# Performance work log

Hardware: AMD Instinct MI355X
Metric: run time of the kernel (lower is better)

The kernel has to match this reference:

```python
import jax, jax.numpy as jnp
from jax import lax
import numpy as np

B = 262144
CLASSES = 11


def setup_inputs() -> dict:
    key = jax.random.key(0)
    ks = jax.random.split(key, 8)
    exponents = jax.random.randint(ks[0], (B, 16), 0, CLASSES, dtype=jnp.int32)
    conv0_w = jax.random.normal(ks[1], (4, 12, 1, 2), jnp.float32) * 0.1
    conv0_b = jax.random.normal(ks[2], (4,), jnp.float32) * 0.05
    conv1_w = jax.random.normal(ks[3], (4, 12, 2, 1), jnp.float32) * 0.1
    # xavier-uniform linears, bias filled with 0.01 (as in init_weights)
    lim1 = float(np.sqrt(6.0 / (96 + 256)))
    linear_w = jax.random.uniform(ks[4], (256, 96), jnp.float32, -lim1, lim1)
    linear_b = jnp.full((256,), 0.01, jnp.float32)
    lim2 = float(np.sqrt(6.0 / (256 + 4)))
    out_w = jax.random.uniform(ks[5], (4, 256), jnp.float32, -lim2, lim2)
    out_b = jnp.full((4,), 0.01, jnp.float32)
    return {"exponents": exponents, "conv0_w": conv0_w, "conv0_b": conv0_b,
            "conv1_w": conv1_w, "linear_w": linear_w, "linear_b": linear_b,
            "out_w": out_w, "out_b": out_b}


def _conv(x, w):
    return lax.conv_general_dilated(x, w, (1, 1), 'VALID',
                                    dimension_numbers=('NCHW', 'OIHW', 'NCHW'))


def _forward(exponents, conv0_w, conv0_b, conv1_w, linear_w, linear_b, out_w, out_b):
    e = exponents.reshape(-1, 4, 4)
    # reconstruct board values: 0 tile stays 0, else 2**e
    x = jnp.where(e == 0, 0.0, jnp.exp2(e.astype(jnp.float32)))  # [B,4,4]
    # rotate_normalize: flips chosen from argmax corner (computed BEFORE flipping)
    corners = jnp.stack([x[:, 0, 0], x[:, 0, -1], x[:, -1, 0], x[:, -1, -1]], axis=1)
    ix = jnp.argmax(corners, axis=1)
    flip_v = ix >= 2          # floor(ix/2) == 1
    flip_h = (ix % 2) == 1
    x = jnp.where(flip_v[:, None, None], x[:, ::-1, :], x)
    x = jnp.where(flip_h[:, None, None], x[:, :, ::-1], x)
    # log2 with 0 -> 0, one-hot over 11 classes
    x_log = jnp.log2(x + (x == 0).astype(jnp.float32))
    onehot = jax.nn.one_hot(jnp.round(x_log).astype(jnp.int32), CLASSES,
                            dtype=jnp.float32)          # [B,4,4,11]
    onehot = jnp.transpose(onehot, (0, 3, 1, 2))         # [B,11,4,4]
    mask = onehot.sum(axis=1, keepdims=True)             # channel 0 (all ones)
    feat = jnp.concatenate([mask, onehot], axis=1)       # [B,12,4,4]
    zh = jax.nn.relu(_conv(feat, conv0_w) + conv0_b[None, :, None, None])  # [B,4,4,3]
    zv = jax.nn.relu(_conv(feat, conv1_w))                                  # [B,4,3,4]
    z1 = jnp.concatenate([zh.reshape(-1, 48), zv.reshape(-1, 48)], axis=1)  # [B,96]
    z2 = jax.nn.relu(z1 @ linear_w.T + linear_b)                            # [B,256]
    probs = jax.nn.softmax(z2 @ out_w.T + out_b, axis=1)                    # [B,4]
    # unscramble: vert swaps actions (0,1); horiz swaps actions (2,3)
    perm = jnp.stack([jnp.where(flip_v, 1, 0), jnp.where(flip_v, 0, 1),
                      jnp.where(flip_h, 3, 2), jnp.where(flip_h, 2, 3)], axis=1)
    return jnp.take_along_axis(probs, perm, axis=1)


def reference(exponents, conv0_w, conv0_b, conv1_w, linear_w, linear_b, out_w, out_b):
    return _forward(exponents, conv0_w, conv0_b, conv1_w, linear_w, linear_b, out_w, out_b)
```

## Files before the change

### kernel.cpp

```cpp
#include <hip/hip_runtime.h>

typedef unsigned int  u32;
typedef unsigned short u16;

typedef float    f4  __attribute__((ext_vector_type(4)));
typedef short    bf8 __attribute__((ext_vector_type(8)));
typedef __fp16   h8  __attribute__((ext_vector_type(8)));
typedef __fp16   h2  __attribute__((ext_vector_type(2)));

#define NBLK  1024
#define ITERS 4
#define ZSTR  104

__device__ __forceinline__ u32 bfr(float f) {
    union { float f; u32 u; } v; v.f = f;
    return (v.u + 0x8000u) >> 16;
}
__device__ __forceinline__ u32 pk2(float lo, float hi) { return bfr(lo) | (bfr(hi) << 16); }
__device__ __forceinline__ u32 pkh(float lo, float hi) {
    union { h2 h; u32 u; } v; v.h = __builtin_amdgcn_cvt_pkrtz(lo, hi); return v.u;
}
__device__ __forceinline__ u32 nrev(u32 x) {
    return ((x >> 12) & 0xFu) | ((x >> 4) & 0xF0u) | ((x << 4) & 0xF00u) | ((x << 12) & 0xF000u);
}

__device__ __forceinline__ void phase1_fn(const int4 e4, u16* __restrict__ z1b, u32* __restrict__ flgb,
                                          const uint2* __restrict__ Th, const uint2* __restrict__ Tv,
                                          const int w, const int m, const int qd)
{
    u32 pkd = (u32)e4.x | ((u32)e4.y << 4) | ((u32)e4.z << 8) | ((u32)e4.w << 12);
    u32 R0 = (u32)__shfl((int)pkd, m);
    u32 R1 = (u32)__shfl((int)pkd, m + 16);
    u32 R2 = (u32)__shfl((int)pkd, m + 32);
    u32 R3 = (u32)__shfl((int)pkd, m + 48);
    u32 c0v = R0 & 15u, c1v = (R0 >> 12) & 15u, c2v = R3 & 15u, c3v = (R3 >> 12) & 15u;
    u32 best = c0v; int ix = 0;
    if (c1v > best) { best = c1v; ix = 1; }
    if (c2v > best) { best = c2v; ix = 2; }
    if (c3v > best) { best = c3v; ix = 3; }
    const bool fv = (ix >= 2), fh = ((ix & 1) != 0);
    u32 F[4];
    F[0] = fv ? R3 : R0;
    F[1] = fv ? R2 : R1;
    F[2] = fv ? R1 : R2;
    F[3] = fv ? R0 : R3;
    #pragma unroll
    for (int i = 0; i < 4; ++i) F[i] = fh ? nrev(F[i]) : F[i];

    if (qd == 0) flgb[w*16 + m] = (u32)fv | ((u32)fh << 1);

    const u32 Fq = F[qd];
    u32 nbq[4], nbc[4];
    #pragma unroll
    for (int j = 0; j < 4; ++j) nbq[j] = (Fq >> (4*j)) & 15u;
    #pragma unroll
    for (int i = 0; i < 4; ++i) nbc[i] = (F[i] >> (4*qd)) & 15u;

    uint2 H0 = Th[nbq[0]*11u + nbq[1]];
    uint2 H1 = Th[nbq[1]*11u + nbq[2]];
    uint2 H2 = Th[nbq[2]*11u + nbq[3]];
    uint2 V0 = Tv[nbc[0]*11u + nbc[1]];
    uint2 V1 = Tv[nbc[1]*11u + nbc[2]];
    uint2 V2 = Tv[nbc[2]*11u + nbc[3]];

    u16* zrow = &z1b[(w*16 + m) * ZSTR];
    *(uint2*)(zrow + (qd*3 + 0)*4) = H0;
    *(uint2*)(zrow + (qd*3 + 1)*4) = H1;
    *(uint2*)(zrow + (qd*3 + 2)*4) = H2;
    *(uint2*)(zrow + 48 + (0*4 + qd)*4) = V0;
    *(uint2*)(zrow + 48 + (1*4 + qd)*4) = V1;
    *(uint2*)(zrow + 48 + (2*4 + qd)*4) = V2;
}

__device__ __forceinline__ void gemm_fn(const u16* __restrict__ z1b, float4* __restrict__ Pb,
                                        const bf8 (&af)[4][3], const u32 (&owA)[2][4], const f4 (&lb4)[4],
                                        const int w, const int m, const int qd)
{
    #pragma unroll
    for (int G = 0; G < 4; ++G) {
        bf8 zb[3];
        #pragma unroll
        for (int s = 0; s < 3; ++s)
            zb[s] = *(const bf8*)(&z1b[(G*16 + m)*ZSTR + s*32 + qd*8]);

        f4 acc_t[4] = {lb4[0], lb4[1], lb4[2], lb4[3]};
        #pragma unroll
        for (int s = 0; s < 3; ++s)
            #pragma unroll
            for (int tt = 0; tt < 4; ++tt)
                acc_t[tt] = __builtin_amdgcn_mfma_f32_16x16x32_bf16(af[tt][s], zb[s], acc_t[tt], 0, 0, 0);

        f4 acc2 = {0.f, 0.f, 0.f, 0.f};
        #pragma unroll
        for (int c = 0; c < 2; ++c) {
            union { u32 u[4]; h8 v; } bu, au;
            bu.u[0] = pkh(fmaxf(acc_t[2*c  ][0], 0.f), fmaxf(acc_t[2*c  ][1], 0.f));
            bu.u[1] = pkh(fmaxf(acc_t[2*c  ][2], 0.f), fmaxf(acc_t[2*c  ][3], 0.f));
            bu.u[2] = pkh(fmaxf(acc_t[2*c+1][0], 0.f), fmaxf(acc_t[2*c+1][1], 0.f));
            bu.u[3] = pkh(fmaxf(acc_t[2*c+1][2], 0.f), fmaxf(acc_t[2*c+1][3], 0.f));
            au.u[0] = owA[c][0]; au.u[1] = owA[c][1]; au.u[2] = owA[c][2]; au.u[3] = owA[c][3];
            acc2 = __builtin_amdgcn_mfma_f32_16x16x32_f16(au.v, bu.v, acc2, 0, 0, 0);
        }
        if (qd == 0)
            Pb[(G*4 + w)*16 + m] = make_float4(acc2[0], acc2[1], acc2[2], acc2[3]);
    }
}

__device__ __forceinline__ void epi_fn(const float4* __restrict__ Pb, const u32 fl, const float4 obv,
                                       float* __restrict__ out, const int base, const int m, const int qd)
{
    float4 s0 = Pb[(qd*4 + 0)*16 + m], s1 = Pb[(qd*4 + 1)*16 + m];
    float4 s2 = Pb[(qd*4 + 2)*16 + m], s3 = Pb[(qd*4 + 3)*16 + m];
    float L0 = s0.x + s1.x + s2.x + s3.x + obv.x;
    float L1 = s0.y + s1.y + s2.y + s3.y + obv.y;
    float L2 = s0.z + s1.z + s2.z + s3.z + obv.z;
    float L3 = s0.w + s1.w + s2.w + s3.w + obv.w;
    float mx = fmaxf(fmaxf(L0, L1), fmaxf(L2, L3));
    float e0 = __expf(L0 - mx), e1 = __expf(L1 - mx), e2 = __expf(L2 - mx), e3 = __expf(L3 - mx);
    float inv = __builtin_amdgcn_rcpf(e0 + e1 + e2 + e3);
    float p0 = e0 * inv, p1 = e1 * inv, p2 = e2 * inv, p3 = e3 * inv;
    float4 o;
    o.x = (fl & 1u) ? p1 : p0;
    o.y = (fl & 1u) ? p0 : p1;
    o.z = (fl & 2u) ? p3 : p2;
    o.w = (fl & 2u) ? p2 : p3;
    *(float4*)(out + (size_t)(base + qd*16 + m) * 4) = o;
}

__launch_bounds__(256, 4)
__global__ void smartcnn_fused(const int* __restrict__ exps,
                               const float* __restrict__ c0w, const float* __restrict__ c0b,
                               const float* __restrict__ c1w,
                               const float* __restrict__ lw,  const float* __restrict__ lb,
                               const float* __restrict__ ow,  const float* __restrict__ ob,
                               float* __restrict__ out)
{
    __shared__ uint2  ThA[121];
    __shared__ uint2  TvA[121];
    __shared__ u16    z1A[64 * ZSTR];
    __shared__ u16    z1B[64 * ZSTR];
    __shared__ float4 PbA[4*4*16];
    __shared__ float4 PbB[4*4*16];
    __shared__ u32    flgA[64];
    __shared__ u32    flgB[64];

    const int tid  = threadIdx.x;
    const int w    = tid >> 6;
    const int lane = tid & 63;
    const int m    = lane & 15;
    const int qd   = lane >> 4;

    for (int i = tid; i < 121; i += 256) {
        int v1 = i / 11, v2 = i - v1 * 11;
        float hv[4], vv[4];
        #pragma unroll
        for (int c = 0; c < 4; ++c) {
            hv[c] = fmaxf(c0w[c*24 + 0] + c0w[c*24 + (1+v1)*2 + 0] + c0b[c]
                        + c0w[c*24 + 1] + c0w[c*24 + (1+v2)*2 + 1], 0.f);
            vv[c] = fmaxf(c1w[c*24 + 0] + c1w[c*24 + (1+v1)*2 + 0]
                        + c1w[c*24 + 1] + c1w[c*24 + (1+v2)*2 + 1], 0.f);
        }
        ThA[i] = make_uint2(pk2(hv[0], hv[1]), pk2(hv[2], hv[3]));
        TvA[i] = make_uint2(pk2(vv[0], vv[1]), pk2(vv[2], vv[3]));
    }

    bf8 af[4][3];
    {
        u16* srow = &z1A[(w*16 + m) * ZSTR];
        #pragma unroll
        for (int tt = 0; tt < 4; ++tt) {
            const int tbase = ((tt & 1) ? 4 : 0) + ((tt >> 1) ? 32 : 0);
            const int fid = 64*w + tbase + 8*(m >> 2) + (m & 3);
            const float* rowp = lw + (size_t)fid*96 + qd*24;
            #pragma unroll
            for (int v = 0; v < 6; ++v) {
                float4 x = *(const float4*)(rowp + v*4);
                u16 e[4] = {(u16)bfr(x.x), (u16)bfr(x.y), (u16)bfr(x.z), (u16)bfr(x.w)};
                #pragma unroll
                for (int j = 0; j < 4; ++j) {
                    int ko = qd*24 + v*4 + j;
                    int kp = (ko < 48) ? ((ko % 12)*4 + ko/12)
                                       : (48 + ((ko - 48) % 12)*4 + (ko - 48)/12);
                    srow[kp] = e[j];
                }
            }
            #pragma unroll
            for (int s = 0; s < 3; ++s)
                af[tt][s] = *(const bf8*)(srow + s*32 + qd*8);
        }
    }
    u32 owA[2][4];
    #pragma unroll
    for (int c = 0; c < 2; ++c) {
        int n8 = 64*w + 32*c + qd*8;
        #pragma unroll
        for (int k = 0; k < 4; ++k)
            owA[c][k] = (m < 4) ? pkh(ow[m*256 + n8 + 2*k], ow[m*256 + n8 + 2*k + 1]) : 0u;
    }
    f4 lb4[4];
    #pragma unroll
    for (int tt = 0; tt < 4; ++tt) {
        const int tbase = ((tt & 1) ? 4 : 0) + ((tt >> 1) ? 32 : 0);
        lb4[tt] = *(const f4*)(lb + 64*w + tbase + 8*qd);
    }
    const float4 obv = *(const float4*)ob;

    const int b0 = blockIdx.x * (ITERS * 64);
    __syncthreads();

    int4 e4 = *(const int4*)(exps + (size_t)(b0 + w*16 + m)*16 + qd*4);
    phase1_fn(e4, z1A, flgA, &ThA[0], &TvA[0], w, m, qd);
    e4 = *(const int4*)(exps + (size_t)(b0 + 64 + w*16 + m)*16 + qd*4);
    __syncthreads();

    #pragma unroll
    for (int itp = 0; itp < ITERS/2; ++itp) {
        const int it = itp * 2;

        const u32 flA = flgA[qd*16 + m];
        phase1_fn(e4, z1B, flgB, &ThA[0], &TvA[0], w, m, qd);
        if (it + 2 < ITERS)
            e4 = *(const int4*)(exps + (size_t)(b0 + (it+2)*64 + w*16 + m)*16 + qd*4);
        gemm_fn(z1A, PbA, af, owA, lb4, w, m, qd);

        __syncthreads();

        const u32 flB = flgB[qd*16 + m];
        if (it + 2 < ITERS) {
            phase1_fn(e4, z1A, flgA, &ThA[0], &TvA[0], w, m, qd);
            if (it + 3 < ITERS)
                e4 = *(const int4*)(exps + (size_t)(b0 + (it+3)*64 + w*16 + m)*16 + qd*4);
        }
        epi_fn(PbA, flA, obv, out, b0 + it*64, m, qd);
        gemm_fn(z1B, PbB, af, owA, lb4, w, m, qd);

        __syncthreads();

        epi_fn(PbB, flB, obv, out, b0 + (it+1)*64, m, qd);
    }
}

extern "C" void kernel_launch(void* const* d_in, const int* in_sizes, int n_in,
                              void* d_out, int out_size, void* d_ws, size_t ws_size,
                              hipStream_t stream) {
    const int*   exps = (const int*)  d_in[0];
    const float* c0w  = (const float*)d_in[1];
    const float* c0b  = (const float*)d_in[2];
    const float* c1w  = (const float*)d_in[3];
    const float* lw   = (const float*)d_in[4];
    const float* lbv  = (const float*)d_in[5];
    const float* oww  = (const float*)d_in[6];
    const float* obv  = (const float*)d_in[7];
    smartcnn_fused<<<NBLK, 256, 0, stream>>>(exps, c0w, c0b, c1w, lw, lbv, oww, obv, (float*)d_out);
}
```

Measured before the change: 102.0 us.

## Double block to 8 waves and specialize producer/consumer warp roles

Launches 512 threads per block and splits the 256 hidden units across 8 waves, so each wave holds half the weight fragments and issues half the MFMAs per tile. Waves 0-3 run the board decode/lookup phase while waves 4-7 run the softmax epilogue, with all waves sharing the GEMM. The aim is to cut per-wave register pressure and serial work and to overlap stages. In exchange the partial-sum buffers double, the epilogue reduces 8 partials instead of 4, and the loop becomes fully unrolled straight-line code.

```diff
diff --git a/kernel.cpp b/kernel.cpp
--- a/kernel.cpp
+++ b/kernel.cpp
@@ -26,7 +26,7 @@
 
 __device__ __forceinline__ void phase1_fn(const int4 e4, u16* __restrict__ z1b, u32* __restrict__ flgb,
                                           const uint2* __restrict__ Th, const uint2* __restrict__ Tv,
-                                          const int w, const int m, const int qd)
+                                          const int pw, const int m, const int qd)
 {
     u32 pkd = (u32)e4.x | ((u32)e4.y << 4) | ((u32)e4.z << 8) | ((u32)e4.w << 12);
     u32 R0 = (u32)__shfl((int)pkd, m);
@@ -47,7 +47,7 @@
     #pragma unroll
     for (int i = 0; i < 4; ++i) F[i] = fh ? nrev(F[i]) : F[i];
 
-    if (qd == 0) flgb[w*16 + m] = (u32)fv | ((u32)fh << 1);
+    if (qd == 0) flgb[pw*16 + m] = (u32)fv | ((u32)fh << 1);
 
     const u32 Fq = F[qd];
     u32 nbq[4], nbc[4];
@@ -63,7 +63,7 @@
     uint2 V1 = Tv[nbc[1]*11u + nbc[2]];
     uint2 V2 = Tv[nbc[2]*11u + nbc[3]];
 
-    u16* zrow = &z1b[(w*16 + m) * ZSTR];
+    u16* zrow = &z1b[(pw*16 + m) * ZSTR];
     *(uint2*)(zrow + (qd*3 + 0)*4) = H0;
     *(uint2*)(zrow + (qd*3 + 1)*4) = H1;
     *(uint2*)(zrow + (qd*3 + 2)*4) = H2;
@@ -73,7 +73,7 @@
 }
 
 __device__ __forceinline__ void gemm_fn(const u16* __restrict__ z1b, float4* __restrict__ Pb,
-                                        const bf8 (&af)[4][3], const u32 (&owA)[2][4], const f4 (&lb4)[4],
+                                        const bf8 (&af)[2][3], const u32 (&owA)[4], const f4 (&lb4)[2],
                                         const int w, const int m, const int qd)
 {
     #pragma unroll
@@ -83,38 +83,35 @@
         for (int s = 0; s < 3; ++s)
             zb[s] = *(const bf8*)(&z1b[(G*16 + m)*ZSTR + s*32 + qd*8]);
 
-        f4 acc_t[4] = {lb4[0], lb4[1], lb4[2], lb4[3]};
+        f4 acc_t[2] = {lb4[0], lb4[1]};
         #pragma unroll
         for (int s = 0; s < 3; ++s)
             #pragma unroll
-            for (int tt = 0; tt < 4; ++tt)
+            for (int tt = 0; tt < 2; ++tt)
                 acc_t[tt] = __builtin_amdgcn_mfma_f32_16x16x32_bf16(af[tt][s], zb[s], acc_t[tt], 0, 0, 0);
 
+        union { u32 u[4]; h8 v; } bu, au;
+        bu.u[0] = pkh(fmaxf(acc_t[0][0], 0.f), fmaxf(acc_t[0][1], 0.f));
+        bu.u[1] = pkh(fmaxf(acc_t[0][2], 0.f), fmaxf(acc_t[0][3], 0.f));
+        bu.u[2] = pkh(fmaxf(acc_t[1][0], 0.f), fmaxf(acc_t[1][1], 0.f));
+        bu.u[3] = pkh(fmaxf(acc_t[1][2], 0.f), fmaxf(acc_t[1][3], 0.f));
+        au.u[0] = owA[0]; au.u[1] = owA[1]; au.u[2] = owA[2]; au.u[3] = owA[3];
         f4 acc2 = {0.f, 0.f, 0.f, 0.f};
-        #pragma unroll
-        for (int c = 0; c < 2; ++c) {
-            union { u32 u[4]; h8 v; } bu, au;
-            bu.u[0] = pkh(fmaxf(acc_t[2*c  ][0], 0.f), fmaxf(acc_t[2*c  ][1], 0.f));
-            bu.u[1] = pkh(fmaxf(acc_t[2*c  ][2], 0.f), fmaxf(acc_t[2*c  ][3], 0.f));
-            bu.u[2] = pkh(fmaxf(acc_t[2*c+1][0], 0.f), fmaxf(acc_t[2*c+1][1], 0.f));
-            bu.u[3] = pkh(fmaxf(acc_t[2*c+1][2], 0.f), fmaxf(acc_t[2*c+1][3], 0.f));
-            au.u[0] = owA[c][0]; au.u[1] = owA[c][1]; au.u[2] = owA[c][2]; au.u[3] = owA[c][3];
-            acc2 = __builtin_amdgcn_mfma_f32_16x16x32_f16(au.v, bu.v, acc2, 0, 0, 0);
-        }
+        acc2 = __builtin_amdgcn_mfma_f32_16x16x32_f16(au.v, bu.v, acc2, 0, 0, 0);
         if (qd == 0)
-            Pb[(G*4 + w)*16 + m] = make_float4(acc2[0], acc2[1], acc2[2], acc2[3]);
+            Pb[(G*8 + w)*16 + m] = make_float4(acc2[0], acc2[1], acc2[2], acc2[3]);
     }
 }
 
 __device__ __forceinline__ void epi_fn(const float4* __restrict__ Pb, const u32 fl, const float4 obv,
                                        float* __restrict__ out, const int base, const int m, const int qd)
 {
-    float4 s0 = Pb[(qd*4 + 0)*16 + m], s1 = Pb[(qd*4 + 1)*16 + m];
-    float4 s2 = Pb[(qd*4 + 2)*16 + m], s3 = Pb[(qd*4 + 3)*16 + m];
-    float L0 = s0.x + s1.x + s2.x + s3.x + obv.x;
-    float L1 = s0.y + s1.y + s2.y + s3.y + obv.y;
-    float L2 = s0.z + s1.z + s2.z + s3.z + obv.z;
-    float L3 = s0.w + s1.w + s2.w + s3.w + obv.w;
+    float L0 = obv.x, L1 = obv.y, L2 = obv.z, L3 = obv.w;
+    #pragma unroll
+    for (int p = 0; p < 8; ++p) {
+        float4 s = Pb[(qd*8 + p)*16 + m];
+        L0 += s.x; L1 += s.y; L2 += s.z; L3 += s.w;
+    }
     float mx = fmaxf(fmaxf(L0, L1), fmaxf(L2, L3));
     float e0 = __expf(L0 - mx), e1 = __expf(L1 - mx), e2 = __expf(L2 - mx), e3 = __expf(L3 - mx);
     float inv = __builtin_amdgcn_rcpf(e0 + e1 + e2 + e3);
@@ -127,7 +124,7 @@
     *(float4*)(out + (size_t)(base + qd*16 + m) * 4) = o;
 }
 
-__launch_bounds__(256, 4)
+__launch_bounds__(512, 4)
 __global__ void smartcnn_fused(const int* __restrict__ exps,
                                const float* __restrict__ c0w, const float* __restrict__ c0b,
                                const float* __restrict__ c1w,
@@ -139,8 +136,8 @@
     __shared__ uint2  TvA[121];
     __shared__ u16    z1A[64 * ZSTR];
     __shared__ u16    z1B[64 * ZSTR];
-    __shared__ float4 PbA[4*4*16];
-    __shared__ float4 PbB[4*4*16];
+    __shared__ float4 PbA[32 * 16];
+    __shared__ float4 PbB[32 * 16];
     __shared__ u32    flgA[64];
     __shared__ u32    flgB[64];
 
@@ -149,8 +146,9 @@
     const int lane = tid & 63;
     const int m    = lane & 15;
     const int qd   = lane >> 4;
-
-    for (int i = tid; i < 121; i += 256) {
+    const bool isP = (w < 4);
+
+    for (int i = tid; i < 121; i += 512) {
         int v1 = i / 11, v2 = i - v1 * 11;
         float hv[4], vv[4];
         #pragma unroll
@@ -164,13 +162,12 @@
         TvA[i] = make_uint2(pk2(vv[0], vv[1]), pk2(vv[2], vv[3]));
     }
 
-    bf8 af[4][3];
+    bf8 af[2][3];
     {
-        u16* srow = &z1A[(w*16 + m) * ZSTR];
-        #pragma unroll
-        for (int tt = 0; tt < 4; ++tt) {
-            const int tbase = ((tt & 1) ? 4 : 0) + ((tt >> 1) ? 32 : 0);
-            const int fid = 64*w + tbase + 8*(m >> 2) + (m & 3);
+        u16* srow = isP ? &z1A[(w*16 + m) * ZSTR] : &z1B[((w-4)*16 + m) * ZSTR];
+        #pragma unroll
+        for (int tt = 0; tt < 2; ++tt) {
+            const int fid = 32*w + 8*(m >> 2) + (m & 3) + 4*tt;
             const float* rowp = lw + (size_t)fid*96 + qd*24;
             #pragma unroll
             for (int v = 0; v < 6; ++v) {
@@ -189,55 +186,65 @@
                 af[tt][s] = *(const bf8*)(srow + s*32 + qd*8);
         }
     }
-    u32 owA[2][4];
-    #pragma unroll
-    for (int c = 0; c < 2; ++c) {
-        int n8 = 64*w + 32*c + qd*8;
-        #pragma unroll
-        for (int k = 0; k < 4; ++k)
-            owA[c][k] = (m < 4) ? pkh(ow[m*256 + n8 + 2*k], ow[m*256 + n8 + 2*k + 1]) : 0u;
-    }
-    f4 lb4[4];
-    #pragma unroll
-    for (int tt = 0; tt < 4; ++tt) {
-        const int tbase = ((tt & 1) ? 4 : 0) + ((tt >> 1) ? 32 : 0);
-        lb4[tt] = *(const f4*)(lb + 64*w + tbase + 8*qd);
-    }
+    u32 owA[4];
+    #pragma unroll
+    for (int k = 0; k < 4; ++k)
+        owA[k] = (m < 4) ? pkh(ow[m*256 + 32*w + 8*qd + 2*k], ow[m*256 + 32*w + 8*qd + 2*k + 1]) : 0u;
+    f4 lb4[2];
+    lb4[0] = *(const f4*)(lb + 32*w + 8*qd);
+    lb4[1] = *(const f4*)(lb + 32*w + 8*qd + 4);
     const float4 obv = *(const float4*)ob;
 
     const int b0 = blockIdx.x * (ITERS * 64);
     __syncthreads();
 
-    int4 e4 = *(const int4*)(exps + (size_t)(b0 + w*16 + m)*16 + qd*4);
-    phase1_fn(e4, z1A, flgA, &ThA[0], &TvA[0], w, m, qd);
-    e4 = *(const int4*)(exps + (size_t)(b0 + 64 + w*16 + m)*16 + qd*4);
-    __syncthreads();
-
-    #pragma unroll
-    for (int itp = 0; itp < ITERS/2; ++itp) {
-        const int it = itp * 2;
-
-        const u32 flA = flgA[qd*16 + m];
+    int4 e4;
+    if (isP) {
+        e4 = *(const int4*)(exps + (size_t)(b0 + w*16 + m)*16 + qd*4);
+        phase1_fn(e4, z1A, flgA, &ThA[0], &TvA[0], w, m, qd);
+        e4 = *(const int4*)(exps + (size_t)(b0 + 64 + w*16 + m)*16 + qd*4);
+    }
+    __syncthreads();
+
+    u32 flA = 0, flB = 0;
+
+    if (isP) {
         phase1_fn(e4, z1B, flgB, &ThA[0], &TvA[0], w, m, qd);
-        if (it + 2 < ITERS)
-            e4 = *(const int4*)(exps + (size_t)(b0 + (it+2)*64 + w*16 + m)*16 + qd*4);
-        gemm_fn(z1A, PbA, af, owA, lb4, w, m, qd);
-
-        __syncthreads();
-
-        const u32 flB = flgB[qd*16 + m];
-        if (it + 2 < ITERS) {
-            phase1_fn(e4, z1A, flgA, &ThA[0], &TvA[0], w, m, qd);
-            if (it + 3 < ITERS)
-                e4 = *(const int4*)(exps + (size_t)(b0 + (it+3)*64 + w*16 + m)*16 + qd*4);
-        }
-        epi_fn(PbA, flA, obv, out, b0 + it*64, m, qd);
-        gemm_fn(z1B, PbB, af, owA, lb4, w, m, qd);
-
-        __syncthreads();
-
-        epi_fn(PbB, flB, obv, out, b0 + (it+1)*64, m, qd);
-    }
+        e4 = *(const int4*)(exps + (size_t)(b0 + 2*64 + w*16 + m)*16 + qd*4);
+    } else {
+        flA = flgA[qd*16 + m];
+    }
+    gemm_fn(z1A, PbA, af, owA, lb4, w, m, qd);
+    __syncthreads();
+
+    if (isP) {
+        phase1_fn(e4, z1A, flgA, &ThA[0], &TvA[0], w, m, qd);
+        e4 = *(const int4*)(exps + (size_t)(b0 + 3*64 + w*16 + m)*16 + qd*4);
+    } else {
+        epi_fn(PbA, flA, obv, out, b0 + 0*64, m, qd);
+        flB = flgB[qd*16 + m];
+    }
+    gemm_fn(z1B, PbB, af, owA, lb4, w, m, qd);
+    __syncthreads();
+
+    if (isP) {
+        phase1_fn(e4, z1B, flgB, &ThA[0], &TvA[0], w, m, qd);
+    } else {
+        epi_fn(PbB, flB, obv, out, b0 + 1*64, m, qd);
+        flA = flgA[qd*16 + m];
+    }
+    gemm_fn(z1A, PbA, af, owA, lb4, w, m, qd);
+    __syncthreads();
+
+    if (!isP) {
+        epi_fn(PbA, flA, obv, out, b0 + 2*64, m, qd);
+        flB = flgB[qd*16 + m];
+    }
+    gemm_fn(z1B, PbB, af, owA, lb4, w, m, qd);
+    __syncthreads();
+
+    if (!isP)
+        epi_fn(PbB, flB, obv, out, b0 + 3*64, m, qd);
 }
 
 extern "C" void kernel_launch(void* const* d_in, const int* in_sizes, int n_in,
@@ -251,5 +258,5 @@
     const float* lbv  = (const float*)d_in[5];
     const float* oww  = (const float*)d_in[6];
     const float* obv  = (const float*)d_in[7];
-    smartcnn_fused<<<NBLK, 256, 0, stream>>>(exps, c0w, c0b, c1w, lw, lbv, oww, obv, (float*)d_out);
-}
+    smartcnn_fused<<<NBLK, 512, 0, stream>>>(exps, c0w, c0b, c1w, lw, lbv, oww, obv, (float*)d_out);
+}
```

After: 108.0 us. +5.9%, slower.
